# Kernel tuning notes

Measured on AMD Instinct MI355X. Metric: run time of the kernel, lower is better.

The kernel has to match this reference:

```python
import jax, jax.numpy as jnp
import numpy as np

# dimensions (match init_kwargs / input_specs)
K = 25        # number of observation events
N_PER = 2048  # observations per event
B = 4096      # batch (sample_idx length)
D = 64        # input_dim
NDIM = 8      # memory_dim
H = D * NDIM  # hidden = 512
STEPS = 2     # euler ODE steps between consecutive obs_times
DT = 0.01
LOG_SQRT_2PI = 0.9189385332046727  # log(sqrt(2*pi))


def _xavier(key, shape):
    lim = np.sqrt(6.0 / (shape[0] + shape[1])).astype(np.float32)
    return jax.random.uniform(key, shape, jnp.float32, -lim, lim)


def setup_inputs() -> dict:
    key = jax.random.key(0)
    ks = jax.random.split(key, 10)
    # unique per-event indices (matches torch scatter-assign semantics)
    rng = np.random.RandomState(0)
    batch_idx = jnp.asarray(
        np.stack([rng.permutation(B)[:N_PER] for _ in range(K)]).reshape(-1),
        jnp.int32)
    return {
        "obs_times": jnp.arange(1, K + 1, dtype=jnp.float32) * (STEPS * DT),
        "event_pt": jnp.arange(K + 1, dtype=jnp.int32) * N_PER,
        "sample_idx": jnp.arange(B, dtype=jnp.int32),
        "X": jax.random.normal(ks[0], (K * N_PER, D), jnp.float32),
        "M": (jax.random.uniform(ks[1], (K * N_PER, D)) < 0.8).astype(jnp.float32),
        "batch_idx": batch_idx,
        # ODEFunc: Linear(H,H) -> Tanh -> Linear(H,H)
        "W_ode1": _xavier(ks[2], (H, H)), "b_ode1": jnp.zeros((H,), jnp.float32),
        "W_ode2": _xavier(ks[3], (H, H)), "b_ode2": jnp.zeros((H,), jnp.float32),
        # GRUCell(D, H)
        "W_ih": _xavier(ks[4], (3 * H, D)), "W_hh": _xavier(ks[5], (3 * H, H)),
        "b_ih": jnp.zeros((3 * H,), jnp.float32), "b_hh": jnp.zeros((3 * H,), jnp.float32),
        # p_model: Linear(H,H) -> ReLU -> (dropout=0) -> Linear(H, 2D)
        "Wp1": _xavier(ks[6], (H, H)), "bp1": jnp.zeros((H,), jnp.float32),
        "Wp2": _xavier(ks[7], (2 * D, H)), "bp2": jnp.zeros((2 * D,), jnp.float32),
    }


def reference(obs_times, event_pt, sample_idx, X, M, batch_idx,
              W_ode1, b_ode1, W_ode2, b_ode2,
              W_ih, W_hh, b_ih, b_hh, Wp1, bp1, Wp2, bp2):
    Xr = X.reshape(K, N_PER, D)
    Mr = M.reshape(K, N_PER, D)
    idx = batch_idx.reshape(K, N_PER)

    def ode_func(h):  # Linear -> Tanh -> Linear
        return jnp.tanh(h @ W_ode1.T + b_ode1) @ W_ode2.T + b_ode2

    def gru(x, h):  # torch GRUCell
        gi = x @ W_ih.T + b_ih
        gh = h @ W_hh.T + b_hh
        i_r, i_z, i_n = jnp.split(gi, 3, axis=1)
        h_r, h_z, h_n = jnp.split(gh, 3, axis=1)
        r = jax.nn.sigmoid(i_r + h_r)
        z = jax.nn.sigmoid(i_z + h_z)
        n = jnp.tanh(i_n + r * h_n)
        return (1.0 - z) * n + z * h

    def event_step(carry, inp):
        h, loss, m_tot = carry
        X_obs, M_obs, i_obs = inp
        # euler odeint over [0, dt], STEPS times to reach obs_time
        for _ in range(STEPS):
            h = h + DT * ode_func(h)
        # likelihood head on all samples, gather observed ones
        p = jax.nn.relu(h @ Wp1.T + bp1) @ Wp2.T + bp2       # [B, 2D]
        p_obs = p[i_obs]                                      # [N_PER, 2D]
        mean, logvar = jnp.split(p_obs, 2, axis=1)
        sigma = jnp.exp(0.5 * logvar)
        error = (X_obs - mean) / sigma
        losses = 0.5 * ((error * error + logvar + 2.0 * LOG_SQRT_2PI) * M_obs)
        # GRU update only on observed indices (scatter)
        h = h.at[i_obs].set(gru(X_obs, h[i_obs]))
        return (h, loss + losses.sum(), m_tot + M_obs.sum()), None

    h0 = jnp.zeros((B, H), jnp.float32)
    (h, loss, m_tot), _ = jax.lax.scan(event_step, (h0, jnp.float32(0.0), jnp.float32(0.0)), (Xr, Mr, idx))
    return (loss / m_tot, jnp.float32(0.0))
```

## Files before the change

kernel.cpp:

```cpp
#include <hip/hip_runtime.h>
#include <cstdint>
#include <cstddef>

#define BATCH 4096
#define DIM 64
#define HID 512
#define NPER 2048
#define KEV 25
#define DT_C 0.01f
#define LOG_SQRT_2PI_C 0.9189385332046727f

typedef __attribute__((ext_vector_type(8))) short short8;
typedef __attribute__((ext_vector_type(4))) float f32x4;

#define MFMA(a, b, c) __builtin_amdgcn_mfma_f32_16x16x32_bf16(a, b, c, 0, 0, 0)
#define BARRIER() __builtin_amdgcn_s_barrier()
#define SCHED0()  __builtin_amdgcn_sched_barrier(0)

__device__ __forceinline__ ushort f2bf(float f) {
    uint32_t u = __float_as_uint(f);
    u += 0x7FFF + ((u >> 16) & 1);
    return (ushort)(u >> 16);
}
__device__ __forceinline__ float sigmoidf_(float x) { return 1.0f / (1.0f + expf(-x)); }

__device__ __forceinline__ void gload_lds16(const ushort* g, ushort* l) {
    __builtin_amdgcn_global_load_lds(
        (const __attribute__((address_space(1))) void*)g,
        (__attribute__((address_space(3))) void*)l, 16, 0, 0);
}
__device__ __forceinline__ void wait_vm(int n) {
    if (n == 8)      asm volatile("s_waitcnt vmcnt(8)" ::: "memory");
    else if (n == 6) asm volatile("s_waitcnt vmcnt(6)" ::: "memory");
    else if (n == 4) asm volatile("s_waitcnt vmcnt(4)" ::: "memory");
    else             asm volatile("s_waitcnt vmcnt(0)" ::: "memory");
}

__device__ __forceinline__ short8 frag64(const ushort* lds, int row, int ks, int lane) {
    int slot = ((ks << 2) + (lane >> 4)) ^ (row & 7);
    return *(const short8*)&lds[row * 64 + slot * 8];
}
__device__ __forceinline__ short8 frag128(const ushort* lds, int row, int ks, int lane) {
    int slot = ((ks << 2) + (lane >> 4)) ^ (row & 7);
    return *(const short8*)&lds[row * 128 + slot * 8];
}

__device__ __forceinline__ void stage128(
    const ushort* g, int row0, int k0, int w, int lane, ushort* lds)
{
    #pragma unroll
    for (int gg = 0; gg < 4; ++gg) {
        int row = row0 + w * 16 + gg * 4 + (lane >> 4);
        int slot = (lane & 15) ^ (row & 7);
        gload_lds16(g + (size_t)row * HID + k0 + slot * 8,
                    &lds[(w * 16 + gg * 4) * 128]);
    }
}

__device__ __forceinline__ void gemm_bk128(
    ushort* A0, ushort* A1, ushort* B0, ushort* B1,
    int w, int lane, int wr, int wc,
    const ushort* Ag, int arow0, const ushort* Bg, int brow0,
    f32x4 acc[2][2])
{
    stage128(Ag, arow0, 0, w, lane, A0);
    stage128(Bg, brow0, 0, w, lane, B0);
    stage128(Ag, arow0, 128, w, lane, A1);
    stage128(Bg, brow0, 128, w, lane, B1);
    for (int t = 0; t < 4; ++t) {
        wait_vm((t < 3) ? 8 : 0);
        BARRIER();
        SCHED0();
        const ushort* Ab = (t & 1) ? A1 : A0;
        const ushort* Bb = (t & 1) ? B1 : B0;
        short8 af[2][4], bf[2][4];
        #pragma unroll
        for (int mi = 0; mi < 2; ++mi) {
            int r = wr * 32 + mi * 16 + (lane & 15);
            #pragma unroll
            for (int ks = 0; ks < 4; ++ks) af[mi][ks] = frag128(Ab, r, ks, lane);
        }
        #pragma unroll
        for (int ni = 0; ni < 2; ++ni) {
            int c = wc * 32 + ni * 16 + (lane & 15);
            #pragma unroll
            for (int ks = 0; ks < 4; ++ks) bf[ni][ks] = frag128(Bb, c, ks, lane);
        }
        #pragma unroll
        for (int ks = 0; ks < 4; ++ks)
            #pragma unroll
            for (int mi = 0; mi < 2; ++mi)
                #pragma unroll
                for (int ni = 0; ni < 2; ++ni)
                    acc[mi][ni] = MFMA(af[mi][ks], bf[ni][ks], acc[mi][ni]);
        SCHED0();
        BARRIER();
        if (t + 2 < 4) {
            stage128(Ag, arow0, (t + 2) * 128, w, lane, (t & 1) ? A1 : A0);
            stage128(Bg, brow0, (t + 2) * 128, w, lane, (t & 1) ? B1 : B0);
        }
    }
}

__global__ __launch_bounds__(256) void fuse1(
    const ushort* __restrict__ hb, const ushort* __restrict__ W1,
    const float* __restrict__ b1, ushort* __restrict__ tbb,
    const ushort* __restrict__ hgb, const ushort* __restrict__ Wp1,
    const float* __restrict__ bp1, ushort* __restrict__ qb, int mode)
{
    __shared__ __align__(16) ushort smem[32768];
    ushort* A0 = smem;         ushort* A1 = smem + 8192;
    ushort* B0 = smem + 16384; ushort* B1 = smem + 24576;
    const int tid = threadIdx.x, lane = tid & 63, w = tid >> 6;
    const int wr = w >> 1, wc = w & 1;
    const int bid = blockIdx.x;

    bool isQ; int b;
    if (mode == 2)      { isQ = true;  b = bid; }
    else if (bid < 512) { isQ = false; b = bid; }
    else                { isQ = true;  b = bid - 512; }
    const ushort* A = isQ ? hgb : hb;
    const ushort* W = isQ ? Wp1 : W1;
    const float* bias = isQ ? bp1 : b1;
    const int r0 = (b >> 3) * 64, c0 = (b & 7) * 64;

    f32x4 acc[2][2] = {};
    gemm_bk128(A0, A1, B0, B1, w, lane, wr, wc, A, r0, W, c0, acc);

    #pragma unroll
    for (int mi = 0; mi < 2; ++mi)
        #pragma unroll
        for (int ni = 0; ni < 2; ++ni) {
            const int c = c0 + wc * 32 + ni * 16 + (lane & 15);
            const float bv = bias[c];
            #pragma unroll
            for (int ii = 0; ii < 4; ++ii) {
                const int r = r0 + wr * 32 + mi * 16 + ((lane >> 4) << 2) + ii;
                const size_t o = (size_t)r * HID + c;
                float v = acc[mi][ni][ii] + bv;
                if (!isQ) tbb[o] = f2bf(tanhf(v));
                else      qb[o]  = f2bf(fmaxf(v, 0.0f));
            }
        }
}

__global__ __launch_bounds__(256) void fuse2(
    const ushort* __restrict__ tbb, const ushort* __restrict__ W2,
    const float* __restrict__ b2, float* __restrict__ h, ushort* __restrict__ hb,
    const int* __restrict__ inv, ushort* __restrict__ hgb,
    const ushort* __restrict__ qb, const ushort* __restrict__ Wp2,
    const float* __restrict__ bp2, const float* __restrict__ Xp,
    const float* __restrict__ Mp, float* __restrict__ sums, int mode)
{
    __shared__ __align__(16) ushort smem[32768];
    const int tid = threadIdx.x, lane = tid & 63, w = tid >> 6;
    const int wr = w >> 1, wc = w & 1;
    const int bid = blockIdx.x;

    bool isP; int b;
    if (mode == 2)      { isP = true;  b = bid; }
    else if (bid < 512) { isP = false; b = bid; }
    else                { isP = true;  b = bid - 512; }

    if (!isP) {
        ushort* A0 = smem;         ushort* A1 = smem + 8192;
        ushort* B0 = smem + 16384; ushort* B1 = smem + 24576;
        const int r0 = (b >> 3) * 64, c0 = (b & 7) * 64;
        f32x4 acc[2][2] = {};
        gemm_bk128(A0, A1, B0, B1, w, lane, wr, wc, tbb, r0, W2, c0, acc);
        #pragma unroll
        for (int mi = 0; mi < 2; ++mi)
            #pragma unroll
            for (int ni = 0; ni < 2; ++ni) {
                const int c = c0 + wc * 32 + ni * 16 + (lane & 15);
                const float bv = b2[c];
                #pragma unroll
                for (int ii = 0; ii < 4; ++ii) {
                    const int r = r0 + wr * 32 + mi * 16 + ((lane >> 4) << 2) + ii;
                    const size_t o = (size_t)r * HID + c;
                    float nh = h[o] + DT_C * (acc[mi][ni][ii] + bv);
                    h[o] = nh;
                    ushort bv16 = f2bf(nh);
                    hb[o] = bv16;
                    if (inv) {
                        int iv = inv[r];
                        if (iv >= 0) hgb[(size_t)iv * HID + c] = bv16;
                    }
                }
            }
        return;
    }

    ushort* A0 = smem;        ushort* A1 = smem + 4096;
    ushort* B0 = smem + 8192; ushort* B1 = smem + 16384;
    const int srow = lane >> 3, sg = ((lane & 7) ^ srow) << 3;
    const int r0t = b * 64;
    const int arow = w * 16 + srow;

    auto stage = [&](int bb, int k0) {
        ushort* A = bb ? A1 : A0; ushort* B = bb ? B1 : B0;
        gload_lds16(qb + (size_t)(r0t + arow) * HID + k0 + sg, &A[(w * 16) * 64]);
        gload_lds16(qb + (size_t)(r0t + arow + 8) * HID + k0 + sg, &A[(w * 16 + 8) * 64]);
        #pragma unroll
        for (int j = 0; j < 4; ++j) {
            int g = w * 4 + j;
            int rw = g * 8 + srow;
            gload_lds16(Wp2 + (size_t)rw * HID + k0 + (((lane & 7) ^ (rw & 7)) << 3),
                        &B[g * 8 * 64]);
        }
    };
    f32x4 acc[2][4] = {};
    stage(0, 0);
    stage(1, 64);
    for (int t = 0; t < 8; ++t) {
        wait_vm((t < 7) ? 6 : 0);
        BARRIER();
        SCHED0();
        const ushort* Ab = (t & 1) ? A1 : A0;
        const ushort* Bb = (t & 1) ? B1 : B0;
        short8 af[2][2], bf[4][2];
        #pragma unroll
        for (int mi = 0; mi < 2; ++mi) {
            int r = wr * 32 + mi * 16 + (lane & 15);
            af[mi][0] = frag64(Ab, r, 0, lane);
            af[mi][1] = frag64(Ab, r, 1, lane);
        }
        #pragma unroll
        for (int ni = 0; ni < 4; ++ni) {
            int c = wc * 64 + ni * 16 + (lane & 15);
            bf[ni][0] = frag64(Bb, c, 0, lane);
            bf[ni][1] = frag64(Bb, c, 1, lane);
        }
        #pragma unroll
        for (int ks = 0; ks < 2; ++ks)
            #pragma unroll
            for (int mi = 0; mi < 2; ++mi)
                #pragma unroll
                for (int ni = 0; ni < 4; ++ni)
                    acc[mi][ni] = MFMA(af[mi][ks], bf[ni][ks], acc[mi][ni]);
        SCHED0();
        BARRIER();
        if (t + 2 < 8) stage(t & 1, (t + 2) * 64);
    }

    float* Plds = (float*)smem;
    #pragma unroll
    for (int mi = 0; mi < 2; ++mi)
        #pragma unroll
        for (int ni = 0; ni < 4; ++ni) {
            int c = wc * 64 + ni * 16 + (lane & 15);
            float bv = bp2[c];
            #pragma unroll
            for (int ii = 0; ii < 4; ++ii) {
                int r = wr * 32 + mi * 16 + ((lane >> 4) << 2) + ii;
                Plds[r * 128 + c] = acc[mi][ni][ii] + bv;
            }
        }
    __syncthreads();

    float local = 0.0f;
    for (int t = tid; t < 64 * 64; t += 256) {
        int r = t >> 6, jj = t & 63;
        float mean = Plds[r * 128 + jj];
        float lv   = Plds[r * 128 + 64 + jj];
        int g = r0t + r;
        float err = (Xp[(size_t)g * 64 + jj] - mean) * expf(-0.5f * lv);
        local += 0.5f * (err * err + lv + 2.0f * LOG_SQRT_2PI_C) * Mp[(size_t)g * 64 + jj];
    }
    #pragma unroll
    for (int o = 32; o > 0; o >>= 1) local += __shfl_down(local, o);
    if (lane == 0) atomicAdd(sums, local);
}

__global__ __launch_bounds__(256) void gru_all(
    const ushort* __restrict__ hgb, const ushort* __restrict__ Xbk,
    const int* __restrict__ idx,
    const ushort* __restrict__ Whh, const ushort* __restrict__ Wih,
    const float* __restrict__ bih, const float* __restrict__ bhh,
    float* __restrict__ h, ushort* __restrict__ hb)
{
    __shared__ __align__(16) ushort smem[32768];
    const int tid = threadIdx.x, lane = tid & 63, w = tid >> 6;
    const int wr = w >> 1, wc = w & 1;
    const int srow = lane >> 3, sg = ((lane & 7) ^ srow) << 3;
    const int bid = blockIdx.x;
    const int r0t = (bid >> 3) * 64, c0 = (bid & 7) * 64;

    auto stage = [&](int b, int p) {
        ushort* A = smem + b * 4096;
        if (p < 8) {
            gload_lds16(hgb + (size_t)(r0t + w * 16 + srow) * HID + p * 64 + sg,
                        &A[(w * 16) * 64]);
            gload_lds16(hgb + (size_t)(r0t + w * 16 + 8 + srow) * HID + p * 64 + sg,
                        &A[(w * 16 + 8) * 64]);
            #pragma unroll
            for (int g = 0; g < 3; ++g) {
                ushort* B = smem + 8192 + (b * 3 + g) * 4096;
                gload_lds16(Whh + (size_t)(g * 512 + c0 + w * 16 + srow) * HID + p * 64 + sg,
                            &B[(w * 16) * 64]);
                gload_lds16(Whh + (size_t)(g * 512 + c0 + w * 16 + 8 + srow) * HID + p * 64 + sg,
                            &B[(w * 16 + 8) * 64]);
            }
        } else {
            gload_lds16(Xbk + (size_t)(r0t + w * 16 + srow) * DIM + sg, &A[(w * 16) * 64]);
            gload_lds16(Xbk + (size_t)(r0t + w * 16 + 8 + srow) * DIM + sg, &A[(w * 16 + 8) * 64]);
            #pragma unroll
            for (int g = 0; g < 3; ++g) {
                ushort* B = smem + 8192 + (b * 3 + g) * 4096;
                gload_lds16(Wih + (size_t)(g * 512 + c0 + w * 16 + srow) * DIM + sg,
                            &B[(w * 16) * 64]);
                gload_lds16(Wih + (size_t)(g * 512 + c0 + w * 16 + 8 + srow) * DIM + sg,
                            &B[(w * 16 + 8) * 64]);
            }
        }
    };

    f32x4 aR[2][2] = {}, aZ[2][2] = {}, aNh[2][2] = {}, aNx[2][2] = {};
    stage(0, 0);
    stage(1, 1);
    for (int t = 0; t < 8; ++t) {
        wait_vm(8);
        BARRIER();
        SCHED0();
        const ushort* Ab = smem + (t & 1) * 4096;
        short8 af[2][2];
        #pragma unroll
        for (int mi = 0; mi < 2; ++mi) {
            int r = wr * 32 + mi * 16 + (lane & 15);
            af[mi][0] = frag64(Ab, r, 0, lane);
            af[mi][1] = frag64(Ab, r, 1, lane);
        }
        #pragma unroll
        for (int g = 0; g < 3; ++g) {
            const ushort* Bb = smem + 8192 + ((t & 1) * 3 + g) * 4096;
            short8 bf[2][2];
            #pragma unroll
            for (int ni = 0; ni < 2; ++ni) {
                int c = wc * 32 + ni * 16 + (lane & 15);
                bf[ni][0] = frag64(Bb, c, 0, lane);
                bf[ni][1] = frag64(Bb, c, 1, lane);
            }
            #pragma unroll
            for (int ks = 0; ks < 2; ++ks)
                #pragma unroll
                for (int mi = 0; mi < 2; ++mi)
                    #pragma unroll
                    for (int ni = 0; ni < 2; ++ni) {
                        f32x4& a = (g == 0) ? aR[mi][ni] : (g == 1) ? aZ[mi][ni] : aNh[mi][ni];
                        a = MFMA(af[mi][ks], bf[ni][ks], a);
                    }
        }
        SCHED0();
        BARRIER();
        if (t + 2 < 9) stage(t & 1, t + 2);
    }
    {
        wait_vm(0);
        BARRIER();
        SCHED0();
        const ushort* Ab = smem;
        short8 af[2][2];
        #pragma unroll
        for (int mi = 0; mi < 2; ++mi) {
            int r = wr * 32 + mi * 16 + (lane & 15);
            af[mi][0] = frag64(Ab, r, 0, lane);
            af[mi][1] = frag64(Ab, r, 1, lane);
        }
        #pragma unroll
        for (int g = 0; g < 3; ++g) {
            const ushort* Bb = smem + 8192 + g * 4096;
            short8 bf[2][2];
            #pragma unroll
            for (int ni = 0; ni < 2; ++ni) {
                int c = wc * 32 + ni * 16 + (lane & 15);
                bf[ni][0] = frag64(Bb, c, 0, lane);
                bf[ni][1] = frag64(Bb, c, 1, lane);
            }
            #pragma unroll
            for (int ks = 0; ks < 2; ++ks)
                #pragma unroll
                for (int mi = 0; mi < 2; ++mi)
                    #pragma unroll
                    for (int ni = 0; ni < 2; ++ni) {
                        f32x4& a = (g == 0) ? aR[mi][ni] : (g == 1) ? aZ[mi][ni] : aNx[mi][ni];
                        a = MFMA(af[mi][ks], bf[ni][ks], a);
                    }
        }
    }

    #pragma unroll
    for (int mi = 0; mi < 2; ++mi)
        #pragma unroll
        for (int ni = 0; ni < 2; ++ni) {
            const int c = c0 + wc * 32 + ni * 16 + (lane & 15);
            const float bR = bih[c] + bhh[c];
            const float bZ = bih[512 + c] + bhh[512 + c];
            const float bNx = bih[1024 + c], bNh = bhh[1024 + c];
            #pragma unroll
            for (int ii = 0; ii < 4; ++ii) {
                const int iobs = r0t + wr * 32 + mi * 16 + ((lane >> 4) << 2) + ii;
                const int gr = idx[iobs];
                float r = sigmoidf_(aR[mi][ni][ii] + bR);
                float z = sigmoidf_(aZ[mi][ni][ii] + bZ);
                float n = tanhf(aNx[mi][ni][ii] + bNx + r * (aNh[mi][ni][ii] + bNh));
                const size_t o = (size_t)gr * HID + c;
                float nh = (1.0f - z) * n + z * h[o];
                h[o] = nh;
                hb[o] = f2bf(nh);
            }
        }
}

__device__ __forceinline__ void block_atomic_sum(float v, float* acc) {
    __shared__ float red[4];
    #pragma unroll
    for (int off = 32; off > 0; off >>= 1) v += __shfl_down(v, off);
    int lane = threadIdx.x & 63, wid = threadIdx.x >> 6;
    if (lane == 0) red[wid] = v;
    __syncthreads();
    if (threadIdx.x == 0) atomicAdd(acc, red[0] + red[1] + red[2] + red[3]);
}

__global__ __launch_bounds__(256) void f2b4_kernel(
    const float* __restrict__ s, ushort* __restrict__ d, int n4)
{
    int t = blockIdx.x * 256 + threadIdx.x;
    if (t >= n4) return;
    float4 v = ((const float4*)s)[t];
    ushort4 o; o.x = f2bf(v.x); o.y = f2bf(v.y); o.z = f2bf(v.z); o.w = f2bf(v.w);
    ((ushort4*)d)[t] = o;
}

__global__ __launch_bounds__(256) void msum_kernel(
    const float* __restrict__ M, int n, float* __restrict__ m_acc)
{
    float v = 0.0f;
    for (int t = blockIdx.x * 256 + threadIdx.x; t < n; t += gridDim.x * 256)
        v += M[t];
    block_atomic_sum(v, m_acc);
}

__global__ __launch_bounds__(256) void inv_scatter(
    const int* __restrict__ bidx, int* __restrict__ inv)
{
    int t = blockIdx.x * 256 + threadIdx.x;
    if (t >= KEV * NPER) return;
    int e = t >> 11, i = t & (NPER - 1);
    inv[(size_t)e * BATCH + bidx[t]] = i;
}

__global__ void finalize_kernel(const float* __restrict__ sums, float* __restrict__ out) {
    if (threadIdx.x == 0) { out[0] = sums[0] / sums[1]; out[1] = 0.0f; }
}

extern "C" void kernel_launch(void* const* d_in, const int* in_sizes, int n_in,
                              void* d_out, int out_size, void* d_ws, size_t ws_size,
                              hipStream_t stream) {
    const float* X      = (const float*)d_in[3];
    const float* M      = (const float*)d_in[4];
    const int* batch_idx= (const int*)  d_in[5];
    const float* W_ode1 = (const float*)d_in[6];
    const float* b_ode1 = (const float*)d_in[7];
    const float* W_ode2 = (const float*)d_in[8];
    const float* b_ode2 = (const float*)d_in[9];
    const float* W_ih   = (const float*)d_in[10];
    const float* W_hh   = (const float*)d_in[11];
    const float* b_ih   = (const float*)d_in[12];
    const float* b_hh   = (const float*)d_in[13];
    const float* Wp1    = (const float*)d_in[14];
    const float* bp1    = (const float*)d_in[15];
    const float* Wp2    = (const float*)d_in[16];
    const float* bp2    = (const float*)d_in[17];
    float* out = (float*)d_out;

    float* ws    = (float*)d_ws;
    float* h     = ws;
    float* sums  = h + (size_t)BATCH * HID;
    int*   inv   = (int*)(sums + 16);
    ushort* hb   = (ushort*)(inv + (size_t)KEV * BATCH);
    ushort* tbb  = hb  + (size_t)BATCH * HID;
    ushort* qb   = tbb + (size_t)BATCH * HID;
    ushort* hgb  = qb  + (size_t)NPER * HID;
    ushort* Xb   = hgb + (size_t)NPER * HID;
    ushort* W1b  = Xb  + (size_t)KEV * NPER * DIM;
    ushort* W2b  = W1b + (size_t)HID * HID;
    ushort* Wp1b = W2b + (size_t)HID * HID;
    ushort* Wp2b = Wp1b + (size_t)HID * HID;
    ushort* Wihb = Wp2b + (size_t)2 * DIM * HID;
    ushort* Whhb = Wihb + (size_t)3 * HID * DIM;

    hipMemsetAsync(h,    0, (size_t)BATCH * HID * sizeof(float), stream);
    hipMemsetAsync(hb,   0, (size_t)BATCH * HID * sizeof(ushort), stream);
    hipMemsetAsync(sums, 0, 2 * sizeof(float), stream);
    hipMemsetAsync(inv,  0xFF, (size_t)KEV * BATCH * sizeof(int), stream);

    dim3 blk(256);
    auto cvt = [&](const float* s, ushort* d, size_t n) {
        f2b4_kernel<<<dim3((unsigned)((n / 4 + 255) / 256)), blk, 0, stream>>>(s, d, (int)(n / 4));
    };
    cvt(W_ode1, W1b,  (size_t)HID * HID);
    cvt(W_ode2, W2b,  (size_t)HID * HID);
    cvt(Wp1,    Wp1b, (size_t)HID * HID);
    cvt(Wp2,    Wp2b, (size_t)2 * DIM * HID);
    cvt(W_ih,   Wihb, (size_t)3 * HID * DIM);
    cvt(W_hh,   Whhb, (size_t)3 * HID * HID);
    cvt(X,      Xb,   (size_t)KEV * NPER * DIM);

    msum_kernel<<<1024, blk, 0, stream>>>(M, KEV * NPER * DIM, sums + 1);
    inv_scatter<<<(KEV * NPER + 255) / 256, blk, 0, stream>>>(batch_idx, inv);

    for (int k = 0; k < KEV; ++k) {
        const ushort* Xbk = Xb + (size_t)k * NPER * DIM;
        const int*   idxk = batch_idx + (size_t)k * NPER;
        int* invk = inv + (size_t)k * BATCH;
        const float* Xp = X + (size_t)(k > 0 ? k - 1 : 0) * NPER * DIM;
        const float* Mp = M + (size_t)(k > 0 ? k - 1 : 0) * NPER * DIM;
        const int m1 = (k > 0) ? 1 : 0;

        fuse1<<<dim3(m1 ? 768 : 512), blk, 0, stream>>>(
            hb, W1b, b_ode1, tbb, hgb, Wp1b, bp1, qb, m1);
        fuse2<<<dim3(m1 ? 544 : 512), blk, 0, stream>>>(
            tbb, W2b, b_ode2, h, hb, nullptr, hgb,
            qb, Wp2b, bp2, Xp, Mp, sums, m1);
        fuse1<<<dim3(512), blk, 0, stream>>>(
            hb, W1b, b_ode1, tbb, hgb, Wp1b, bp1, qb, 0);
        fuse2<<<dim3(512), blk, 0, stream>>>(
            tbb, W2b, b_ode2, h, hb, invk, hgb,
            qb, Wp2b, bp2, Xp, Mp, sums, 0);
        gru_all<<<dim3(256), blk, 0, stream>>>(
            hgb, Xbk, idxk, Whhb, Wihb, b_ih, b_hh, h, hb);
    }

    {
        const float* Xp = X + (size_t)(KEV - 1) * NPER * DIM;
        const float* Mp = M + (size_t)(KEV - 1) * NPER * DIM;
        fuse1<<<dim3(256), blk, 0, stream>>>(
            hb, W1b, b_ode1, tbb, hgb, Wp1b, bp1, qb, 2);
        fuse2<<<dim3(32), blk, 0, stream>>>(
            tbb, W2b, b_ode2, h, hb, nullptr, hgb,
            qb, Wp2b, bp2, Xp, Mp, sums, 2);
    }

    finalize_kernel<<<1, 64, 0, stream>>>(sums, out);
}
```

Before: 1.930 ms.

## Halve GRU row tile to 32 and launch twice as many blocks

The GRU kernel now handles 32 observed rows per block instead of 64, so the launch grows from 256 to 512 workgroups. That gives more parallelism on a GPU with many CUs. Each wave now computes a 32x16 column slice for all three gates, and weight staging is redistributed with six 8-row loads per wave. The wait count changes to vmcnt(7) to match the new per-stage load count. In exchange, each weight tile is reused across fewer rows, so total weight traffic from L2 doubles.

After: 1.943 ms. No clear change (+0.7%).

```diff
diff --git a/kernel.cpp b/kernel.cpp
--- a/kernel.cpp
+++ b/kernel.cpp
@@ -31,6 +31,7 @@
 }
 __device__ __forceinline__ void wait_vm(int n) {
     if (n == 8)      asm volatile("s_waitcnt vmcnt(8)" ::: "memory");
+    else if (n == 7) asm volatile("s_waitcnt vmcnt(7)" ::: "memory");
     else if (n == 6) asm volatile("s_waitcnt vmcnt(6)" ::: "memory");
     else if (n == 4) asm volatile("s_waitcnt vmcnt(4)" ::: "memory");
     else             asm volatile("s_waitcnt vmcnt(0)" ::: "memory");
@@ -279,80 +280,68 @@
     const float* __restrict__ bih, const float* __restrict__ bhh,
     float* __restrict__ h, ushort* __restrict__ hb)
 {
-    __shared__ __align__(16) ushort smem[32768];
+    __shared__ __align__(16) ushort smem[28672];
     const int tid = threadIdx.x, lane = tid & 63, w = tid >> 6;
-    const int wr = w >> 1, wc = w & 1;
     const int srow = lane >> 3, sg = ((lane & 7) ^ srow) << 3;
     const int bid = blockIdx.x;
-    const int r0t = (bid >> 3) * 64, c0 = (bid & 7) * 64;
+    const int r0t = (bid >> 3) * 32, c0 = (bid & 7) * 64;
 
     auto stage = [&](int b, int p) {
-        ushort* A = smem + b * 4096;
+        ushort* A = smem + b * 2048;
+        ushort* B = smem + 4096 + b * 12288;
         if (p < 8) {
-            gload_lds16(hgb + (size_t)(r0t + w * 16 + srow) * HID + p * 64 + sg,
-                        &A[(w * 16) * 64]);
-            gload_lds16(hgb + (size_t)(r0t + w * 16 + 8 + srow) * HID + p * 64 + sg,
-                        &A[(w * 16 + 8) * 64]);
-            #pragma unroll
-            for (int g = 0; g < 3; ++g) {
-                ushort* B = smem + 8192 + (b * 3 + g) * 4096;
-                gload_lds16(Whh + (size_t)(g * 512 + c0 + w * 16 + srow) * HID + p * 64 + sg,
-                            &B[(w * 16) * 64]);
-                gload_lds16(Whh + (size_t)(g * 512 + c0 + w * 16 + 8 + srow) * HID + p * 64 + sg,
-                            &B[(w * 16 + 8) * 64]);
+            gload_lds16(hgb + (size_t)(r0t + w * 8 + srow) * HID + p * 64 + sg,
+                        &A[(w * 8) * 64]);
+            #pragma unroll
+            for (int j = 0; j < 6; ++j) {
+                int glid = w * 6 + j;
+                int g = glid >> 3, rg = (glid & 7) * 8 + srow;
+                gload_lds16(Whh + (size_t)(g * 512 + c0 + rg) * HID + p * 64 + sg,
+                            &B[glid * 8 * 64]);
             }
         } else {
-            gload_lds16(Xbk + (size_t)(r0t + w * 16 + srow) * DIM + sg, &A[(w * 16) * 64]);
-            gload_lds16(Xbk + (size_t)(r0t + w * 16 + 8 + srow) * DIM + sg, &A[(w * 16 + 8) * 64]);
-            #pragma unroll
-            for (int g = 0; g < 3; ++g) {
-                ushort* B = smem + 8192 + (b * 3 + g) * 4096;
-                gload_lds16(Wih + (size_t)(g * 512 + c0 + w * 16 + srow) * DIM + sg,
-                            &B[(w * 16) * 64]);
-                gload_lds16(Wih + (size_t)(g * 512 + c0 + w * 16 + 8 + srow) * DIM + sg,
-                            &B[(w * 16 + 8) * 64]);
+            gload_lds16(Xbk + (size_t)(r0t + w * 8 + srow) * DIM + sg, &A[(w * 8) * 64]);
+            #pragma unroll
+            for (int j = 0; j < 6; ++j) {
+                int glid = w * 6 + j;
+                int g = glid >> 3, rg = (glid & 7) * 8 + srow;
+                gload_lds16(Wih + (size_t)(g * 512 + c0 + rg) * DIM + sg,
+                            &B[glid * 8 * 64]);
             }
         }
     };
 
-    f32x4 aR[2][2] = {}, aZ[2][2] = {}, aNh[2][2] = {}, aNx[2][2] = {};
+    f32x4 aR[2] = {}, aZ[2] = {}, aNh[2] = {}, aNx[2] = {};
     stage(0, 0);
     stage(1, 1);
     for (int t = 0; t < 8; ++t) {
-        wait_vm(8);
-        BARRIER();
-        SCHED0();
-        const ushort* Ab = smem + (t & 1) * 4096;
+        wait_vm((t < 7) ? 7 : 7);
+        BARRIER();
+        SCHED0();
+        const ushort* Ab = smem + (t & 1) * 2048;
         short8 af[2][2];
         #pragma unroll
         for (int mi = 0; mi < 2; ++mi) {
-            int r = wr * 32 + mi * 16 + (lane & 15);
+            int r = mi * 16 + (lane & 15);
             af[mi][0] = frag64(Ab, r, 0, lane);
             af[mi][1] = frag64(Ab, r, 1, lane);
         }
+        const int c_l = w * 16 + (lane & 15);
         #pragma unroll
         for (int g = 0; g < 3; ++g) {
-            const ushort* Bb = smem + 8192 + ((t & 1) * 3 + g) * 4096;
-            short8 bf[2][2];
-            #pragma unroll
-            for (int ni = 0; ni < 2; ++ni) {
-                int c = wc * 32 + ni * 16 + (lane & 15);
-                bf[ni][0] = frag64(Bb, c, 0, lane);
-                bf[ni][1] = frag64(Bb, c, 1, lane);
-            }
-            #pragma unroll
-            for (int ks = 0; ks < 2; ++ks)
-                #pragma unroll
-                for (int mi = 0; mi < 2; ++mi)
-                    #pragma unroll
-                    for (int ni = 0; ni < 2; ++ni) {
-                        f32x4& a = (g == 0) ? aR[mi][ni] : (g == 1) ? aZ[mi][ni] : aNh[mi][ni];
-                        a = MFMA(af[mi][ks], bf[ni][ks], a);
-                    }
-        }
-        SCHED0();
-        BARRIER();
-        if (t + 2 < 9) stage(t & 1, t + 2);
+            const ushort* Bb = smem + 4096 + (t & 1) * 12288 + g * 4096;
+            short8 bf0 = frag64(Bb, c_l, 0, lane);
+            short8 bf1 = frag64(Bb, c_l, 1, lane);
+            #pragma unroll
+            for (int mi = 0; mi < 2; ++mi) {
+                f32x4& a = (g == 0) ? aR[mi] : (g == 1) ? aZ[mi] : aNh[mi];
+                a = MFMA(af[mi][0], bf0, a);
+                a = MFMA(af[mi][1], bf1, a);
+            }
+        }
+        SCHED0();
+        BARRIER();
+        if (t + 2 <= 8) stage(t & 1, t + 2);
     }
     {
         wait_vm(0);
@@ -362,53 +351,45 @@
         short8 af[2][2];
         #pragma unroll
         for (int mi = 0; mi < 2; ++mi) {
-            int r = wr * 32 + mi * 16 + (lane & 15);
+            int r = mi * 16 + (lane & 15);
             af[mi][0] = frag64(Ab, r, 0, lane);
             af[mi][1] = frag64(Ab, r, 1, lane);
         }
+        const int c_l = w * 16 + (lane & 15);
         #pragma unroll
         for (int g = 0; g < 3; ++g) {
-            const ushort* Bb = smem + 8192 + g * 4096;
-            short8 bf[2][2];
-            #pragma unroll
-            for (int ni = 0; ni < 2; ++ni) {
-                int c = wc * 32 + ni * 16 + (lane & 15);
-                bf[ni][0] = frag64(Bb, c, 0, lane);
-                bf[ni][1] = frag64(Bb, c, 1, lane);
-            }
-            #pragma unroll
-            for (int ks = 0; ks < 2; ++ks)
-                #pragma unroll
-                for (int mi = 0; mi < 2; ++mi)
-                    #pragma unroll
-                    for (int ni = 0; ni < 2; ++ni) {
-                        f32x4& a = (g == 0) ? aR[mi][ni] : (g == 1) ? aZ[mi][ni] : aNx[mi][ni];
-                        a = MFMA(af[mi][ks], bf[ni][ks], a);
-                    }
-        }
-    }
-
-    #pragma unroll
-    for (int mi = 0; mi < 2; ++mi)
-        #pragma unroll
-        for (int ni = 0; ni < 2; ++ni) {
-            const int c = c0 + wc * 32 + ni * 16 + (lane & 15);
-            const float bR = bih[c] + bhh[c];
-            const float bZ = bih[512 + c] + bhh[512 + c];
-            const float bNx = bih[1024 + c], bNh = bhh[1024 + c];
+            const ushort* Bb = smem + 4096 + g * 4096;
+            short8 bf0 = frag64(Bb, c_l, 0, lane);
+            short8 bf1 = frag64(Bb, c_l, 1, lane);
+            #pragma unroll
+            for (int mi = 0; mi < 2; ++mi) {
+                f32x4& a = (g == 0) ? aR[mi] : (g == 1) ? aZ[mi] : aNx[mi];
+                a = MFMA(af[mi][0], bf0, a);
+                a = MFMA(af[mi][1], bf1, a);
+            }
+        }
+    }
+
+    {
+        const int c = c0 + w * 16 + (lane & 15);
+        const float bR = bih[c] + bhh[c];
+        const float bZ = bih[512 + c] + bhh[512 + c];
+        const float bNx = bih[1024 + c], bNh = bhh[1024 + c];
+        #pragma unroll
+        for (int mi = 0; mi < 2; ++mi)
             #pragma unroll
             for (int ii = 0; ii < 4; ++ii) {
-                const int iobs = r0t + wr * 32 + mi * 16 + ((lane >> 4) << 2) + ii;
+                const int iobs = r0t + mi * 16 + ((lane >> 4) << 2) + ii;
                 const int gr = idx[iobs];
-                float r = sigmoidf_(aR[mi][ni][ii] + bR);
-                float z = sigmoidf_(aZ[mi][ni][ii] + bZ);
-                float n = tanhf(aNx[mi][ni][ii] + bNx + r * (aNh[mi][ni][ii] + bNh));
+                float r = sigmoidf_(aR[mi][ii] + bR);
+                float z = sigmoidf_(aZ[mi][ii] + bZ);
+                float n = tanhf(aNx[mi][ii] + bNx + r * (aNh[mi][ii] + bNh));
                 const size_t o = (size_t)gr * HID + c;
                 float nh = (1.0f - z) * n + z * h[o];
                 h[o] = nh;
                 hb[o] = f2bf(nh);
             }
-        }
+    }
 }
 
 __device__ __forceinline__ void block_atomic_sum(float v, float* acc) {
@@ -527,7 +508,7 @@
         fuse2<<<dim3(512), blk, 0, stream>>>(
             tbb, W2b, b_ode2, h, hb, invk, hgb,
             qb, Wp2b, bp2, Xp, Mp, sums, 0);
-        gru_all<<<dim3(256), blk, 0, stream>>>(
+        gru_all<<<dim3(512), blk, 0, stream>>>(
             hgb, Xbk, idxk, Whhb, Wihb, b_ih, b_hh, h, hb);
     }
 
```
